# Optimization experiments

Hardware: AMD Instinct MI355X
Metric: run time of the kernel (lower is better)

Reference implementation:

```python
import jax, jax.numpy as jnp
import numpy as np

N = 20000      # nodes
E = 160000     # edges (before self loops)
IN = 128       # in_channels (== edge_dim)
H = 8          # heads
C = 64         # out_channels per head
NEG_SLOPE = 0.2


def setup_inputs() -> dict:
    key = jax.random.key(0)
    ks = jax.random.split(key, 8)
    s_in = np.float32(1.0 / np.sqrt(IN))
    s_att = np.float32(1.0 / np.sqrt(C))
    return {
        "x": jax.random.normal(ks[0], (N, IN), jnp.float32),
        "edge_index": jax.random.randint(ks[1], (2, E), 0, N, dtype=jnp.int32),
        "edge_attr": jax.random.normal(ks[2], (E, IN), jnp.float32),
        "Wl": jax.random.normal(ks[3], (IN, H * C), jnp.float32) * s_in,
        "Wr": jax.random.normal(ks[4], (IN, H * C), jnp.float32) * s_in,
        "We": jax.random.normal(ks[5], (IN, H * C), jnp.float32) * s_in,
        "att": jax.random.normal(ks[6], (H, C), jnp.float32) * s_att,
        "bias": jnp.zeros((H * C,), jnp.float32),
    }


def reference(x, edge_index, edge_attr, Wl, Wr, We, att, bias):
    n = x.shape[0]
    e = edge_attr.shape[0]
    src, dst = edge_index[0], edge_index[1]

    # add self loops; self-loop edge_attr = per-target-node mean of incoming
    # edge attrs (PyG fill_value='mean'); nodes with no in-edges get zeros.
    cnt = jax.ops.segment_sum(jnp.ones((e,), x.dtype), dst, num_segments=n)
    loop_attr = jax.ops.segment_sum(edge_attr, dst, num_segments=n) / jnp.maximum(cnt, 1.0)[:, None]
    loops = jnp.arange(n, dtype=src.dtype)
    src_f = jnp.concatenate([src, loops])          # [E+N]
    dst_f = jnp.concatenate([dst, loops])          # [E+N]
    ea = jnp.concatenate([edge_attr, loop_attr], axis=0)  # [E+N, IN]

    xl = (x @ Wl).reshape(n, H, C)   # source projection
    xr = (x @ Wr).reshape(n, H, C)   # target projection
    xe = (ea @ We).reshape(-1, H, C)  # edge projection

    # GATv2 score: att . LeakyReLU(xl_j + xr_i + xe)
    m = jax.nn.leaky_relu(xl[src_f] + xr[dst_f] + xe, NEG_SLOPE)  # [E+N, H, C]
    logits = jnp.einsum('ehc,hc->eh', m, att)                      # [E+N, H]

    # segment softmax over incoming edges of each target node
    lmax = jax.ops.segment_max(logits, dst_f, num_segments=n)      # [N, H]
    p = jnp.exp(logits - lmax[dst_f])
    denom = jax.ops.segment_sum(p, dst_f, num_segments=n)
    alpha = p / denom[dst_f]                                       # [E+N, H]

    # weighted scatter-add aggregation of source features
    out = jax.ops.segment_sum(alpha[:, :, None] * xl[src_f], dst_f, num_segments=n)
    return out.reshape(n, H * C) + bias
```

## Files before the change

kernel.cpp:

```cpp
#include <hip/hip_runtime.h>

#define N_NODES 20000
#define E_EDGES 160000
#define IN_CH 128
#define H_HEADS 8
#define C_CH 64
#define HC 512
#define M_TOT (E_EDGES + N_NODES)
#define NEG_SLOPE 0.2f
#define NCHUNK ((N_NODES + 255) / 256)

typedef __attribute__((ext_vector_type(8))) short bf16x8;
typedef __attribute__((ext_vector_type(4))) short bf16x4;
typedef __attribute__((ext_vector_type(4))) float f32x4;

__device__ __forceinline__ unsigned short f2bf(float f) {
    unsigned u = __float_as_uint(f);
    unsigned r = (u + 0x7FFFu + ((u >> 16) & 1u)) >> 16;
    return (unsigned short)r;
}
__device__ __forceinline__ unsigned short f2bf_trunc(float f) {
    return (unsigned short)(__float_as_uint(f) >> 16);
}
__device__ __forceinline__ float bf2f(unsigned short s) {
    return __uint_as_float((unsigned)s << 16);
}
__device__ __forceinline__ float bfx(const bf16x8& v0, const bf16x8& v1, int idx) {
    return bf2f((unsigned short)((idx < 8) ? v0[idx] : v1[idx - 8]));
}

#define GLOAD_LDS16(gsrc, ldst) \
    __builtin_amdgcn_global_load_lds((const __attribute__((address_space(1))) void*)(gsrc), \
                                     (__attribute__((address_space(3))) void*)(ldst), 16, 0, 0)

__global__ void k_deg(const int* __restrict__ ei, int* __restrict__ deg) {
    int e = blockIdx.x * blockDim.x + threadIdx.x;
    if (e >= E_EDGES) return;
    atomicAdd(&deg[ei[E_EDGES + e]], 1);
}

__global__ void k_scan1(const int* __restrict__ deg, int* __restrict__ bsum) {
    __shared__ int red[256];
    int tid = threadIdx.x;
    int i = blockIdx.x * 256 + tid;
    red[tid] = (i < N_NODES) ? deg[i] + 1 : 0;
    __syncthreads();
    for (int off = 128; off > 0; off >>= 1) {
        if (tid < off) red[tid] += red[tid + off];
        __syncthreads();
    }
    if (tid == 0) bsum[blockIdx.x] = red[0];
}

__global__ void k_scan2(const int* __restrict__ bsum, int* __restrict__ boff) {
    if (threadIdx.x == 0) {
        int run = 0;
        for (int b = 0; b < NCHUNK; ++b) { boff[b] = run; run += bsum[b]; }
    }
}

__global__ void k_scan3(const int* __restrict__ deg, const int* __restrict__ boff,
                        int* __restrict__ rowptr, int* __restrict__ cursor,
                        int4* __restrict__ edat) {
    __shared__ int buf[256];
    int tid = threadIdx.x;
    int i = blockIdx.x * 256 + tid;
    int v = (i < N_NODES) ? deg[i] + 1 : 0;
    buf[tid] = v;
    __syncthreads();
    for (int off = 1; off < 256; off <<= 1) {
        int tv = (tid >= off) ? buf[tid - off] : 0;
        __syncthreads();
        buf[tid] += tv;
        __syncthreads();
    }
    if (i < N_NODES) {
        int excl = boff[blockIdx.x] + buf[tid] - v;
        rowptr[i] = excl;
        edat[excl] = make_int4(E_EDGES + i, i, i, 0);
        cursor[i] = excl + 1;
        if (i == N_NODES - 1) rowptr[N_NODES] = excl + v;
    }
}

__global__ void k_fill(const int* __restrict__ ei, int* __restrict__ cursor,
                       int4* __restrict__ edat) {
    int e = blockIdx.x * blockDim.x + threadIdx.x;
    if (e >= E_EDGES) return;
    int d = ei[E_EDGES + e];
    int slot = atomicAdd(&cursor[d], 1);
    edat[slot] = make_int4(e, ei[e], d, 0);
}

__global__ void k_prep(const int* __restrict__ rowptr, const int4* __restrict__ edat,
                       const float* __restrict__ ea, unsigned short* __restrict__ eab) {
    int node = (blockIdx.x * blockDim.x + threadIdx.x) >> 6;
    int lane = threadIdx.x & 63;
    if (node >= N_NODES) return;
    int beg = rowptr[node], end = rowptr[node + 1];
    int cnt = end - beg - 1;
    float s0 = 0.f, s1 = 0.f;
    if (beg + 1 < end) {
        const float* p_nxt = ea + (size_t)edat[beg + 1].x * 128 + lane;
        for (int p = beg + 1; p < end; ++p) {
            const float* cur = p_nxt;
            if (p + 1 < end) p_nxt = ea + (size_t)edat[p + 1].x * 128 + lane;
            float v0 = cur[0], v1 = cur[64];
            s0 += v0; s1 += v1;
            eab[(size_t)p * 128 + lane] = f2bf(v0);
            eab[(size_t)p * 128 + 64 + lane] = f2bf(v1);
        }
    }
    float inv = 1.f / fmaxf((float)cnt, 1.f);
    eab[(size_t)beg * 128 + lane] = f2bf(s0 * inv);
    eab[(size_t)beg * 128 + 64 + lane] = f2bf(s1 * inv);
}

__global__ void k_trans3(const float* __restrict__ Wl, const float* __restrict__ Wr,
                         const float* __restrict__ We,
                         unsigned short* __restrict__ WlT, unsigned short* __restrict__ WrT,
                         unsigned short* __restrict__ WeT) {
    int idx = blockIdx.x * blockDim.x + threadIdx.x;
    if (idx >= HC * IN_CH) return;
    int m = blockIdx.y;
    const float* W = (m == 0) ? Wl : (m == 1) ? Wr : We;
    unsigned short* WT = (m == 0) ? WlT : (m == 1) ? WrT : WeT;
    int n = idx >> 7, k = idx & 127;
    WT[idx] = f2bf(W[(size_t)k * HC + n]);
}

__global__ void k_gemm2(const float* __restrict__ A,
                        const unsigned short* __restrict__ WlT,
                        const unsigned short* __restrict__ WrT,
                        unsigned short* __restrict__ xlb, unsigned short* __restrict__ xrb,
                        int M) {
    __shared__ short As[64 * 128];
    int row0 = blockIdx.x * 64;
    int sel = blockIdx.y >> 1;
    const unsigned short* BT = sel ? WrT : WlT;
    unsigned short* Cb = sel ? xrb : xlb;
    int t = threadIdx.x;
    {
        int row = t >> 2, c0 = (t & 3) * 32;
        int gr = row0 + row;
        int sw = (row & 7) << 4;
        const float* src = A + (size_t)gr * 128 + c0;
        #pragma unroll
        for (int i = 0; i < 4; ++i) {
            bf16x8 v;
            if (gr < M) {
                const float4* p = (const float4*)(src + i * 8);
                float4 f0 = p[0], f1 = p[1];
                v[0] = f2bf(f0.x); v[1] = f2bf(f0.y); v[2] = f2bf(f0.z); v[3] = f2bf(f0.w);
                v[4] = f2bf(f1.x); v[5] = f2bf(f1.y); v[6] = f2bf(f1.z); v[7] = f2bf(f1.w);
            } else {
                #pragma unroll
                for (int j = 0; j < 8; ++j) v[j] = 0;
            }
            int off = row * 256 + (((c0 + i * 8) * 2) ^ sw);
            *(bf16x8*)((char*)As + off) = v;
        }
    }
    __syncthreads();

    int w = t >> 6, l = t & 63;
    int lr = l & 15, lk = l >> 4;
    int col0 = (blockIdx.y & 1) * 256 + w * 64;

    f32x4 acc[4][4];
    #pragma unroll
    for (int mi = 0; mi < 4; ++mi)
        #pragma unroll
        for (int fj = 0; fj < 4; ++fj)
            #pragma unroll
            for (int q = 0; q < 4; ++q) acc[mi][fj][q] = 0.f;

    #pragma unroll
    for (int k0 = 0; k0 < 4; ++k0) {
        bf16x8 a4[4];
        #pragma unroll
        for (int mi = 0; mi < 4; ++mi) {
            int row = mi * 16 + lr;
            int off = row * 256 + ((k0 * 64 + lk * 16) ^ ((row & 7) << 4));
            a4[mi] = *(const bf16x8*)((const char*)As + off);
        }
        #pragma unroll
        for (int fj = 0; fj < 4; ++fj) {
            bf16x8 b = *(const bf16x8*)(BT + (size_t)(col0 + fj * 16 + lr) * 128 + k0 * 32 + lk * 8);
            #pragma unroll
            for (int mi = 0; mi < 4; ++mi)
                acc[mi][fj] = __builtin_amdgcn_mfma_f32_16x16x32_bf16(a4[mi], b, acc[mi][fj], 0, 0, 0);
        }
    }
    #pragma unroll
    for (int mi = 0; mi < 4; ++mi) {
        #pragma unroll
        for (int reg = 0; reg < 4; ++reg) {
            int r = row0 + mi * 16 + lk * 4 + reg;
            if (r < M) {
                unsigned short* cp = Cb + (size_t)r * 512 + col0 + lr;
                #pragma unroll
                for (int fj = 0; fj < 4; ++fj) cp[fj * 16] = f2bf(acc[mi][fj][reg]);
            }
        }
    }
}

#define PREF(R, CB, SLOT) { \
    int s_ = s_src[R], d_ = s_dst[R]; \
    const bf16x8* xp_ = (const bf16x8*)(xlb + (size_t)s_ * 512 + (CB) + q * 16); \
    pa0[SLOT] = xp_[0]; pa1[SLOT] = xp_[1]; \
    const bf16x8* rp_ = (const bf16x8*)(xrb + (size_t)d_ * 512 + (CB) + q * 16); \
    pb0[SLOT] = rp_[0]; pb1[SLOT] = rp_[1]; }

__global__ void k_fused(const int4* __restrict__ edat, const int* __restrict__ rowptr,
                        const unsigned short* __restrict__ eab,
                        const unsigned short* __restrict__ WeT,
                        const unsigned short* __restrict__ xlb,
                        const unsigned short* __restrict__ xrb,
                        const float* __restrict__ att, const float* __restrict__ bias,
                        float* __restrict__ lq, float* __restrict__ out) {
    __shared__ short As[64 * 128];
    __shared__ unsigned short xeT[4][16][72];
    __shared__ float att_s[256];
    __shared__ float lg[64][4];
    __shared__ int s_src[64], s_dst[64];
    __shared__ int own_node[64], own_beg[64], own_len[64];
    __shared__ int n_own;
    int row0 = blockIdx.x * 64;
    int y = blockIdx.y;
    int t = threadIdx.x;

    if (t == 0) n_own = 0;
    __syncthreads();

    {
        int l = t & 63;
        int c_base = (t >> 6) * 4;
        #pragma unroll
        for (int i = 0; i < 4; ++i) {
            int c = c_base + i;
            int row_local = c * 4 + (l >> 4);
            int grow = row0 + row_local;
            if (grow > M_TOT - 1) grow = M_TOT - 1;
            int chunk = (l & 15) ^ (row_local & 7);
            const char* src = (const char*)eab + (size_t)grow * 256 + chunk * 16;
            char* dst = (char*)As + c * 1024;
            GLOAD_LDS16(src, dst);
        }
    }

    if (t < 64) {
        int p = row0 + t;
        int s = 0, d = 0;
        if (p < M_TOT) {
            int4 v = edat[p];
            s = v.y; d = v.z;
            int pb = rowptr[d], pe = rowptr[d + 1];
            if (pb == p && pe <= row0 + 64) {
                int idx = atomicAdd(&n_own, 1);
                own_node[idx] = d; own_beg[idx] = t; own_len[idx] = pe - pb;
            }
        }
        s_src[t] = s; s_dst[t] = d;
    }
    att_s[t & 255] = att[y * 256 + (t & 255)];

    asm volatile("s_waitcnt vmcnt(0)");
    __syncthreads();

    int w = t >> 6, l = t & 63;
    int lr = l & 15, lk = l >> 4;
    int eloc = l >> 2, q = l & 3;
    int h = y * 4 + w;
    int cb = h * 64;

    bf16x8 pa0[2], pa1[2], pb0[2], pb1[2];
    f32x4 acc[4][4];

    PREF(eloc, cb, 0);

    #pragma unroll
    for (int mi = 0; mi < 4; ++mi)
        #pragma unroll
        for (int fj = 0; fj < 4; ++fj)
            #pragma unroll
            for (int qq = 0; qq < 4; ++qq) acc[mi][fj][qq] = 0.f;

    #pragma unroll
    for (int k0 = 0; k0 < 4; ++k0) {
        bf16x8 a4[4];
        #pragma unroll
        for (int mi = 0; mi < 4; ++mi) {
            int row = mi * 16 + lr;
            int off = row * 256 + ((k0 * 64 + lk * 16) ^ ((row & 7) << 4));
            a4[mi] = *(const bf16x8*)((const char*)As + off);
        }
        #pragma unroll
        for (int fj = 0; fj < 4; ++fj) {
            bf16x8 b = *(const bf16x8*)(WeT + (size_t)(cb + fj * 16 + lr) * 128 + k0 * 32 + lk * 8);
            #pragma unroll
            for (int mi = 0; mi < 4; ++mi)
                acc[mi][fj] = __builtin_amdgcn_mfma_f32_16x16x32_bf16(a4[mi], b, acc[mi][fj], 0, 0, 0);
        }
    }

    #pragma unroll
    for (int mi = 0; mi < 4; ++mi) {
        if (mi < 3) { PREF(mi * 16 + 16 + eloc, cb, (mi + 1) & 1); }

        #pragma unroll
        for (int fj = 0; fj < 4; ++fj)
            #pragma unroll
            for (int reg = 0; reg < 4; ++reg)
                xeT[w][lk * 4 + reg][fj * 16 + lr] = f2bf_trunc(acc[mi][fj][reg]);

        const bf16x8 ca0 = pa0[mi & 1], ca1 = pa1[mi & 1];
        const bf16x8 cb0v = pb0[mi & 1], cb1v = pb1[mi & 1];

        bf16x8 x0 = *(const bf16x8*)&xeT[w][eloc][q * 16];
        bf16x8 x1 = *(const bf16x8*)&xeT[w][eloc][q * 16 + 8];

        float sum = 0.f;
        #pragma unroll
        for (int sg = 0; sg < 4; ++sg) {
            float4 av = *(const float4*)&att_s[w * 64 + q * 16 + sg * 4];
            float v0 = bfx(x0, x1, sg * 4 + 0) + bfx(ca0, ca1, sg * 4 + 0) + bfx(cb0v, cb1v, sg * 4 + 0);
            float v1 = bfx(x0, x1, sg * 4 + 1) + bfx(ca0, ca1, sg * 4 + 1) + bfx(cb0v, cb1v, sg * 4 + 1);
            float v2 = bfx(x0, x1, sg * 4 + 2) + bfx(ca0, ca1, sg * 4 + 2) + bfx(cb0v, cb1v, sg * 4 + 2);
            float v3 = bfx(x0, x1, sg * 4 + 3) + bfx(ca0, ca1, sg * 4 + 3) + bfx(cb0v, cb1v, sg * 4 + 3);
            v0 = (v0 > 0.f) ? v0 : v0 * NEG_SLOPE;
            v1 = (v1 > 0.f) ? v1 : v1 * NEG_SLOPE;
            v2 = (v2 > 0.f) ? v2 : v2 * NEG_SLOPE;
            v3 = (v3 > 0.f) ? v3 : v3 * NEG_SLOPE;
            sum = fmaf(av.x, v0, sum);
            sum = fmaf(av.y, v1, sum);
            sum = fmaf(av.z, v2, sum);
            sum = fmaf(av.w, v3, sum);
        }
        sum += __shfl_xor(sum, 1, 64);
        sum += __shfl_xor(sum, 2, 64);
        if (q == 0) lg[mi * 16 + eloc][w] = sum;
    }
    __syncthreads();

    if (t < 64) {
        int p = row0 + t;
        if (p < M_TOT) {
            const float4* lr4 = (const float4*)&lg[t][0];
            *(float4*)(lq + ((size_t)y * M_TOT + p) * 4) = lr4[0];
        }
    }

    {
        int lane = t & 63;
        int hl = lane >> 4;
        int coff = y * 256 + lane * 4;
        for (int o = w; o < n_own; o += 4) {
            int d = own_node[o], rb = own_beg[o], len = own_len[o];
            float m = -3.4e38f;
            for (int j = 0; j < len; ++j) m = fmaxf(m, lg[rb + j][hl]);
            float den = 0.f;
            for (int j = 0; j < len; ++j) den += __expf(lg[rb + j][hl] - m);
            float rden = 1.f / den;
            float ac[4] = {};
            bf16x4 v_nxt = *(const bf16x4*)(xlb + (size_t)s_src[rb] * 512 + coff);
            for (int j = 0; j < len; ++j) {
                bf16x4 v = v_nxt;
                if (j + 1 < len)
                    v_nxt = *(const bf16x4*)(xlb + (size_t)s_src[rb + j + 1] * 512 + coff);
                float alpha = __expf(lg[rb + j][hl] - m) * rden;
                #pragma unroll
                for (int jj = 0; jj < 4; ++jj) ac[jj] = fmaf(alpha, bf2f((unsigned short)v[jj]), ac[jj]);
            }
            const float4* bp = (const float4*)(bias + coff);
            float4 bv = bp[0];
            float4 r0 = { ac[0] + bv.x, ac[1] + bv.y, ac[2] + bv.z, ac[3] + bv.w };
            *(float4*)(out + (size_t)d * 512 + coff) = r0;
        }
    }
}

__global__ void k_cleanup(const int* __restrict__ rowptr, const int4* __restrict__ edat,
                          const float* __restrict__ lq,
                          const unsigned short* __restrict__ xlb, const float* __restrict__ bias,
                          float* __restrict__ out) {
    int node = (blockIdx.x * blockDim.x + threadIdx.x) >> 6;
    int lane = threadIdx.x & 63;
    if (node >= N_NODES) return;
    int beg = rowptr[node], end = rowptr[node + 1];
    if ((beg >> 6) == ((end - 1) >> 6)) return;
    int h = lane >> 3;
    const float* lp = lq + (size_t)(h >> 2) * M_TOT * 4 + (h & 3);

    float m = -3.4e38f;
    for (int p = beg; p < end; ++p) m = fmaxf(m, lp[(size_t)p * 4]);
    float den = 0.f;
    for (int p = beg; p < end; ++p) den += __expf(lp[(size_t)p * 4] - m);
    float rden = 1.f / den;

    float acc[8] = {};
    bf16x8 v_nxt = *(const bf16x8*)(xlb + (size_t)edat[beg].y * 512 + lane * 8);
    for (int p = beg; p < end; ++p) {
        bf16x8 v = v_nxt;
        float lgv = lp[(size_t)p * 4];
        if (p + 1 < end)
            v_nxt = *(const bf16x8*)(xlb + (size_t)edat[p + 1].y * 512 + lane * 8);
        float alpha = __expf(lgv - m) * rden;
        #pragma unroll
        for (int j = 0; j < 8; ++j) acc[j] = fmaf(alpha, bf2f((unsigned short)v[j]), acc[j]);
    }
    float4* op = (float4*)(out + (size_t)node * 512 + lane * 8);
    const float4* bp = (const float4*)(bias + lane * 8);
    float4 bv0 = bp[0], bv1 = bp[1];
    float4 r0 = { acc[0] + bv0.x, acc[1] + bv0.y, acc[2] + bv0.z, acc[3] + bv0.w };
    float4 r1 = { acc[4] + bv1.x, acc[5] + bv1.y, acc[6] + bv1.z, acc[7] + bv1.w };
    op[0] = r0; op[1] = r1;
}

extern "C" void kernel_launch(void* const* d_in, const int* in_sizes, int n_in,
                              void* d_out, int out_size, void* d_ws, size_t ws_size,
                              hipStream_t stream) {
    const float* x    = (const float*)d_in[0];
    const int*   ei   = (const int*)d_in[1];
    const float* ea   = (const float*)d_in[2];
    const float* Wl   = (const float*)d_in[3];
    const float* Wr   = (const float*)d_in[4];
    const float* We   = (const float*)d_in[5];
    const float* att  = (const float*)d_in[6];
    const float* bias = (const float*)d_in[7];
    float* out = (float*)d_out;

    unsigned short* xlb = (unsigned short*)d_ws;
    unsigned short* xrb = xlb + (size_t)N_NODES * HC;
    unsigned short* WlT = xrb + (size_t)N_NODES * HC;
    unsigned short* WrT = WlT + HC * IN_CH;
    unsigned short* WeT = WrT + HC * IN_CH;
    unsigned short* eab = WeT + HC * IN_CH;
    float* lq        = (float*)(eab + (size_t)M_TOT * IN_CH);
    int4* edat       = (int4*)(lq + (size_t)2 * M_TOT * 4);
    int* deg         = (int*)(edat + M_TOT);
    int* rowptr      = deg + N_NODES;
    int* cursor      = rowptr + N_NODES + 1;
    int* bsum        = cursor + N_NODES;
    int* boff        = bsum + NCHUNK;

    const int B = 256;
    hipMemsetAsync(deg, 0, N_NODES * sizeof(int), stream);
    k_deg<<<(E_EDGES + B - 1) / B, B, 0, stream>>>(ei, deg);
    k_scan1<<<NCHUNK, B, 0, stream>>>(deg, bsum);
    k_scan2<<<1, 64, 0, stream>>>(bsum, boff);
    k_scan3<<<NCHUNK, B, 0, stream>>>(deg, boff, rowptr, cursor, edat);
    k_fill<<<(E_EDGES + B - 1) / B, B, 0, stream>>>(ei, cursor, edat);
    k_prep<<<((size_t)N_NODES * 64 + B - 1) / B, B, 0, stream>>>(rowptr, edat, ea, eab);
    k_trans3<<<dim3((HC * IN_CH + B - 1) / B, 3), B, 0, stream>>>(Wl, Wr, We, WlT, WrT, WeT);
    k_gemm2<<<dim3((N_NODES + 63) / 64, 4), B, 0, stream>>>(x, WlT, WrT, xlb, xrb, N_NODES);
    k_fused<<<dim3((M_TOT + 63) / 64, 2), B, 0, stream>>>(edat, rowptr, eab, WeT,
                                                          xlb, xrb, att, bias, lq, out);
    k_cleanup<<<((size_t)N_NODES * 64 + B - 1) / B, B, 0, stream>>>(rowptr, edat, lq,
                                                                    xlb, bias, out);
}
```

Before: 247.7 us.

## Merge head-half grid dimension into single 512-thread fused block over all heads

After: 232.5 us. 6.1% less time.

```diff
diff --git a/kernel.cpp b/kernel.cpp
--- a/kernel.cpp
+++ b/kernel.cpp
@@ -11,7 +11,6 @@
 #define NCHUNK ((N_NODES + 255) / 256)
 
 typedef __attribute__((ext_vector_type(8))) short bf16x8;
-typedef __attribute__((ext_vector_type(4))) short bf16x4;
 typedef __attribute__((ext_vector_type(4))) float f32x4;
 
 __device__ __forceinline__ unsigned short f2bf(float f) {
@@ -213,22 +212,22 @@
     const bf16x8* rp_ = (const bf16x8*)(xrb + (size_t)d_ * 512 + (CB) + q * 16); \
     pb0[SLOT] = rp_[0]; pb1[SLOT] = rp_[1]; }
 
-__global__ void k_fused(const int4* __restrict__ edat, const int* __restrict__ rowptr,
-                        const unsigned short* __restrict__ eab,
-                        const unsigned short* __restrict__ WeT,
-                        const unsigned short* __restrict__ xlb,
-                        const unsigned short* __restrict__ xrb,
-                        const float* __restrict__ att, const float* __restrict__ bias,
-                        float* __restrict__ lq, float* __restrict__ out) {
+__global__ __launch_bounds__(512, 2)
+void k_fused(const int4* __restrict__ edat, const int* __restrict__ rowptr,
+             const unsigned short* __restrict__ eab,
+             const unsigned short* __restrict__ WeT,
+             const unsigned short* __restrict__ xlb,
+             const unsigned short* __restrict__ xrb,
+             const float* __restrict__ att, const float* __restrict__ bias,
+             float* __restrict__ logits, float* __restrict__ out) {
     __shared__ short As[64 * 128];
-    __shared__ unsigned short xeT[4][16][72];
-    __shared__ float att_s[256];
-    __shared__ float lg[64][4];
+    __shared__ unsigned short xeT[8][16][72];
+    __shared__ float att_s[512];
+    __shared__ float lg[64][8];
     __shared__ int s_src[64], s_dst[64];
     __shared__ int own_node[64], own_beg[64], own_len[64];
     __shared__ int n_own;
     int row0 = blockIdx.x * 64;
-    int y = blockIdx.y;
     int t = threadIdx.x;
 
     if (t == 0) n_own = 0;
@@ -236,9 +235,9 @@
 
     {
         int l = t & 63;
-        int c_base = (t >> 6) * 4;
-        #pragma unroll
-        for (int i = 0; i < 4; ++i) {
+        int c_base = (t >> 6) * 2;
+        #pragma unroll
+        for (int i = 0; i < 2; ++i) {
             int c = c_base + i;
             int row_local = c * 4 + (l >> 4);
             int grow = row0 + row_local;
@@ -264,7 +263,7 @@
         }
         s_src[t] = s; s_dst[t] = d;
     }
-    att_s[t & 255] = att[y * 256 + (t & 255)];
+    att_s[t] = att[t];
 
     asm volatile("s_waitcnt vmcnt(0)");
     __syncthreads();
@@ -272,8 +271,7 @@
     int w = t >> 6, l = t & 63;
     int lr = l & 15, lk = l >> 4;
     int eloc = l >> 2, q = l & 3;
-    int h = y * 4 + w;
-    int cb = h * 64;
+    int cb = w * 64;
 
     bf16x8 pa0[2], pa1[2], pb0[2], pb1[2];
     f32x4 acc[4][4];
@@ -324,7 +322,7 @@
         float sum = 0.f;
         #pragma unroll
         for (int sg = 0; sg < 4; ++sg) {
-            float4 av = *(const float4*)&att_s[w * 64 + q * 16 + sg * 4];
+            float4 av = *(const float4*)&att_s[cb + q * 16 + sg * 4];
             float v0 = bfx(x0, x1, sg * 4 + 0) + bfx(ca0, ca1, sg * 4 + 0) + bfx(cb0v, cb1v, sg * 4 + 0);
             float v1 = bfx(x0, x1, sg * 4 + 1) + bfx(ca0, ca1, sg * 4 + 1) + bfx(cb0v, cb1v, sg * 4 + 1);
             float v2 = bfx(x0, x1, sg * 4 + 2) + bfx(ca0, ca1, sg * 4 + 2) + bfx(cb0v, cb1v, sg * 4 + 2);
@@ -344,45 +342,47 @@
     }
     __syncthreads();
 
-    if (t < 64) {
-        int p = row0 + t;
-        if (p < M_TOT) {
-            const float4* lr4 = (const float4*)&lg[t][0];
-            *(float4*)(lq + ((size_t)y * M_TOT + p) * 4) = lr4[0];
+    {
+        int nval = (M_TOT - row0 < 64 ? M_TOT - row0 : 64) * 8;
+        if (t < 256 && t * 2 < nval) {
+            const float* lf = (const float*)lg;
+            float2 v = { lf[t * 2], lf[t * 2 + 1] };
+            *(float2*)(logits + (size_t)row0 * 8 + t * 2) = v;
         }
     }
 
     {
         int lane = t & 63;
-        int hl = lane >> 4;
-        int coff = y * 256 + lane * 4;
-        for (int o = w; o < n_own; o += 4) {
+        int h = lane >> 3;
+        for (int o = w; o < n_own; o += 8) {
             int d = own_node[o], rb = own_beg[o], len = own_len[o];
             float m = -3.4e38f;
-            for (int j = 0; j < len; ++j) m = fmaxf(m, lg[rb + j][hl]);
+            for (int j = 0; j < len; ++j) m = fmaxf(m, lg[rb + j][h]);
             float den = 0.f;
-            for (int j = 0; j < len; ++j) den += __expf(lg[rb + j][hl] - m);
+            for (int j = 0; j < len; ++j) den += __expf(lg[rb + j][h] - m);
             float rden = 1.f / den;
-            float ac[4] = {};
-            bf16x4 v_nxt = *(const bf16x4*)(xlb + (size_t)s_src[rb] * 512 + coff);
+            float ac[8] = {};
+            bf16x8 v_nxt = *(const bf16x8*)(xlb + (size_t)s_src[rb] * 512 + lane * 8);
             for (int j = 0; j < len; ++j) {
-                bf16x4 v = v_nxt;
+                bf16x8 v = v_nxt;
                 if (j + 1 < len)
-                    v_nxt = *(const bf16x4*)(xlb + (size_t)s_src[rb + j + 1] * 512 + coff);
-                float alpha = __expf(lg[rb + j][hl] - m) * rden;
+                    v_nxt = *(const bf16x8*)(xlb + (size_t)s_src[rb + j + 1] * 512 + lane * 8);
+                float alpha = __expf(lg[rb + j][h] - m) * rden;
                 #pragma unroll
-                for (int jj = 0; jj < 4; ++jj) ac[jj] = fmaf(alpha, bf2f((unsigned short)v[jj]), ac[jj]);
+                for (int jj = 0; jj < 8; ++jj) ac[jj] = fmaf(alpha, bf2f((unsigned short)v[jj]), ac[jj]);
             }
-            const float4* bp = (const float4*)(bias + coff);
-            float4 bv = bp[0];
-            float4 r0 = { ac[0] + bv.x, ac[1] + bv.y, ac[2] + bv.z, ac[3] + bv.w };
-            *(float4*)(out + (size_t)d * 512 + coff) = r0;
+            float4* op = (float4*)(out + (size_t)d * 512 + lane * 8);
+            const float4* bp = (const float4*)(bias + lane * 8);
+            float4 bv0 = bp[0], bv1 = bp[1];
+            float4 r0 = { ac[0] + bv0.x, ac[1] + bv0.y, ac[2] + bv0.z, ac[3] + bv0.w };
+            float4 r1 = { ac[4] + bv1.x, ac[5] + bv1.y, ac[6] + bv1.z, ac[7] + bv1.w };
+            op[0] = r0; op[1] = r1;
         }
     }
 }
 
 __global__ void k_cleanup(const int* __restrict__ rowptr, const int4* __restrict__ edat,
-                          const float* __restrict__ lq,
+                          const float* __restrict__ logits,
                           const unsigned short* __restrict__ xlb, const float* __restrict__ bias,
                           float* __restrict__ out) {
     int node = (blockIdx.x * blockDim.x + threadIdx.x) >> 6;
@@ -391,19 +391,18 @@
     int beg = rowptr[node], end = rowptr[node + 1];
     if ((beg >> 6) == ((end - 1) >> 6)) return;
     int h = lane >> 3;
-    const float* lp = lq + (size_t)(h >> 2) * M_TOT * 4 + (h & 3);
 
     float m = -3.4e38f;
-    for (int p = beg; p < end; ++p) m = fmaxf(m, lp[(size_t)p * 4]);
+    for (int p = beg; p < end; ++p) m = fmaxf(m, logits[(size_t)p * 8 + h]);
     float den = 0.f;
-    for (int p = beg; p < end; ++p) den += __expf(lp[(size_t)p * 4] - m);
+    for (int p = beg; p < end; ++p) den += __expf(logits[(size_t)p * 8 + h] - m);
     float rden = 1.f / den;
 
     float acc[8] = {};
     bf16x8 v_nxt = *(const bf16x8*)(xlb + (size_t)edat[beg].y * 512 + lane * 8);
     for (int p = beg; p < end; ++p) {
         bf16x8 v = v_nxt;
-        float lgv = lp[(size_t)p * 4];
+        float lgv = logits[(size_t)p * 8 + h];
         if (p + 1 < end)
             v_nxt = *(const bf16x8*)(xlb + (size_t)edat[p + 1].y * 512 + lane * 8);
         float alpha = __expf(lgv - m) * rden;
@@ -437,8 +436,8 @@
     unsigned short* WrT = WlT + HC * IN_CH;
     unsigned short* WeT = WrT + HC * IN_CH;
     unsigned short* eab = WeT + HC * IN_CH;
-    float* lq        = (float*)(eab + (size_t)M_TOT * IN_CH);
-    int4* edat       = (int4*)(lq + (size_t)2 * M_TOT * 4);
+    float* logits    = (float*)(eab + (size_t)M_TOT * IN_CH);
+    int4* edat       = (int4*)(logits + (size_t)M_TOT * 8);
     int* deg         = (int*)(edat + M_TOT);
     int* rowptr      = deg + N_NODES;
     int* cursor      = rowptr + N_NODES + 1;
@@ -455,8 +454,8 @@
     k_prep<<<((size_t)N_NODES * 64 + B - 1) / B, B, 0, stream>>>(rowptr, edat, ea, eab);
     k_trans3<<<dim3((HC * IN_CH + B - 1) / B, 3), B, 0, stream>>>(Wl, Wr, We, WlT, WrT, WeT);
     k_gemm2<<<dim3((N_NODES + 63) / 64, 4), B, 0, stream>>>(x, WlT, WrT, xlb, xrb, N_NODES);
-    k_fused<<<dim3((M_TOT + 63) / 64, 2), B, 0, stream>>>(edat, rowptr, eab, WeT,
-                                                          xlb, xrb, att, bias, lq, out);
-    k_cleanup<<<((size_t)N_NODES * 64 + B - 1) / B, B, 0, stream>>>(rowptr, edat, lq,
+    k_fused<<<(M_TOT + 63) / 64, 512, 0, stream>>>(edat, rowptr, eab, WeT,
+                                                   xlb, xrb, att, bias, logits, out);
+    k_cleanup<<<((size_t)N_NODES * 64 + B - 1) / B, B, 0, stream>>>(rowptr, edat, logits,
                                                                     xlb, bias, out);
 }
```
